# Kernel optimization log

Hardware: AMD Instinct MI355X
Metric: run time of the kernel (lower is better)

## Reference

```python
import jax, jax.numpy as jnp
import numpy as np

N = 50000       # nodes
E = 1600000     # directed edges (avg degree 32)
H = 2           # heads (layers 1-2)
F_IN = 128
F_HID = 64      # per-head hidden channels
F_OUT = 64
SCALE = 0.05


def setup_inputs() -> dict:
    key = jax.random.key(0)
    ks = jax.random.split(key, 15)

    def p(k, shape):
        return jax.random.normal(k, shape, jnp.float32) * SCALE

    x = jax.random.normal(ks[0], (N, F_IN), jnp.float32)
    edge_index = jax.random.randint(ks[1], (2, E), 0, N, dtype=jnp.int64)
    return dict(
        x=x,
        W1=p(ks[2], (F_IN, H * F_HID)), as1=p(ks[3], (H, F_HID)), ad1=p(ks[4], (H, F_HID)), b1=p(ks[5], (H * F_HID,)),
        W2=p(ks[6], (H * F_HID, H * F_HID)), as2=p(ks[7], (H, F_HID)), ad2=p(ks[8], (H, F_HID)), b2=p(ks[9], (H * F_HID,)),
        W3=p(ks[10], (H * F_HID, F_OUT)), as3=p(ks[11], (1, F_OUT)), ad3=p(ks[12], (1, F_OUT)), b3=p(ks[13], (F_OUT,)),
        edge_index=edge_index,
    )


def gat_layer(x, W, a_src, a_dst, b, src, dst, heads, f_out):
    """One PyG-style GATConv (concat=True, negative_slope=0.2), dropout off (eval)."""
    n = x.shape[0]
    h = (x @ W).reshape(n, heads, f_out)                 # [N,H,F]
    al_s = jnp.einsum('nhf,hf->nh', h, a_src)            # (x_j * att_src).sum(-1)
    al_d = jnp.einsum('nhf,hf->nh', h, a_dst)
    e = jax.nn.leaky_relu(al_s[src] + al_d[dst], 0.2)    # [Etot,H]
    # segment softmax over incoming edges of each dst node
    m = jax.lax.stop_gradient(jax.ops.segment_max(e, dst, num_segments=n))
    ee = jnp.exp(e - m[dst])
    denom = jax.ops.segment_sum(ee, dst, num_segments=n)
    alpha = ee / (denom[dst] + 1e-16)                    # [Etot,H]
    out = jax.ops.segment_sum(h[src] * alpha[:, :, None], dst, num_segments=n)
    return out.reshape(n, heads * f_out) + b


def reference(x, W1, as1, ad1, b1, W2, as2, ad2, b2, W3, as3, ad3, b3, edge_index):
    # add_self_loops=True (PyG default): same augmented edge set for all layers
    loops = jnp.arange(N, dtype=edge_index.dtype)
    src = jnp.concatenate([edge_index[0], loops])
    dst = jnp.concatenate([edge_index[1], loops])
    h = jax.nn.elu(gat_layer(x, W1, as1, ad1, b1, src, dst, H, F_HID))
    h = jax.nn.elu(gat_layer(h, W2, as2, ad2, b2, src, dst, H, F_HID))
    h = jax.nn.elu(gat_layer(h, W3, as3, ad3, b3, src, dst, 1, F_OUT))
    return h
```

## Files before the change

kernel.cpp:

```cpp
#include <hip/hip_runtime.h>
#include <hip/hip_bf16.h>
#include <hip/hip_fp16.h>


#define ELU(x) ((x) > 0.f ? (x) : (__expf(x) - 1.f))
#define BSH 8
#define CHK 8192

typedef _Float16 f16x8 __attribute__((ext_vector_type(8)));
typedef float    f32x4 __attribute__((ext_vector_type(4)));
typedef float    f32x2 __attribute__((ext_vector_type(2)));

__device__ inline unsigned int f16x4_to_fp8(__half2 h0, __half2 h1) {
    float2 a = __half22float2(h0), b = __half22float2(h1);
    unsigned int r = __builtin_amdgcn_cvt_pk_fp8_f32(a.x, a.y, 0, false);
    r = __builtin_amdgcn_cvt_pk_fp8_f32(b.x, b.y, r, true);
    return r;
}

__global__ __launch_bounds__(256) void phase0(
    const float* __restrict__ W1, __half* __restrict__ Wt1,
    const float* __restrict__ W2, __half* __restrict__ Wt2,
    const float* __restrict__ W3, __half* __restrict__ Wt3,
    const int* __restrict__ ei, int* __restrict__ bhist_rows, int E_)
{
    const int t = threadIdx.x;
    const int b = blockIdx.x;
    if (b < 160) {
        const float* W; __half* Wt; int N, base;
        if (b < 64)       { W = W1; Wt = Wt1; N = 128; base = b; }
        else if (b < 128) { W = W2; Wt = Wt2; N = 128; base = b - 64; }
        else              { W = W3; Wt = Wt3; N = 64;  base = b - 128; }
        int idx = base * 256 + t;
        if (idx < N * 128) {
            int nn = idx >> 7, k = idx & 127;
            Wt[idx] = __float2half(W[k * N + nn]);
        }
    } else {
        __shared__ int cnt[256];
        int hb = b - 160;
        cnt[t] = 0;
        __syncthreads();
        const int e0 = hb * CHK;
        for (int i = t; i < CHK; i += 256) {
            int e = e0 + i;
            if (e >= E_) break;
            atomicAdd(&cnt[ei[E_ + e] >> BSH], 1);
        }
        __syncthreads();
        bhist_rows[hb * 256 + t] = cnt[t];
    }
}

__global__ __launch_bounds__(256) void scan_bases(
    const int* __restrict__ bhist_rows, int* __restrict__ boff,
    int* __restrict__ bases, int* __restrict__ part, int HB, int n, int NB)
{
    __shared__ int tot[256];
    __shared__ int col[256];
    const int t = threadIdx.x;
    const int b = blockIdx.x;

    int v = 0;
    for (int r = 0; r < HB; r++) v += bhist_rows[r * 256 + t];
    int nodes_t = n - (t << BSH);
    nodes_t = nodes_t < 0 ? 0 : (nodes_t > 256 ? 256 : nodes_t);
    v = (t < NB) ? (v + nodes_t) : 0;
    tot[t] = v;
    __syncthreads();
    for (int d = 1; d < 256; d <<= 1) {
        int x = (t >= d) ? tot[t - d] : 0;
        __syncthreads();
        tot[t] += x;
        __syncthreads();
    }
    if (b == 0) {
        if (t < NB) boff[t + 1] = tot[t];
        if (t == 0) boff[0] = 0;
    }
    const int base0 = (b > 0) ? tot[b - 1] : 0;
    const int bend  = tot[b];

    int c = (t < HB) ? bhist_rows[t * 256 + b] : 0;
    col[t] = c;
    __syncthreads();
    for (int d = 1; d < 256; d <<= 1) {
        int x = (t >= d) ? col[t - d] : 0;
        __syncthreads();
        col[t] += x;
        __syncthreads();
    }
    if (t < HB) bases[b * HB + t] = base0 + col[t] - c;

    const int n0 = b << BSH;
    const int nodes = min(256, n - n0);
    const int sl0 = bend - nodes;
    if (t < nodes) part[sl0 + t] = (n0 + t) | (t << 16);
}

__global__ __launch_bounds__(256) void edge_partition(
    const int* __restrict__ ei, const int* __restrict__ bases,
    int* __restrict__ part, int E_, int HB, int NB)
{
    __shared__ int cnt[256];
    __shared__ int sbase[256];
    const int t = threadIdx.x;
    const int hb = blockIdx.x;
    cnt[t] = 0;
    sbase[t] = (t < NB) ? bases[t * HB + hb] : 0;
    __syncthreads();
    const int e0 = hb * CHK;
    for (int i = t; i < CHK; i += 256) {
        int e = e0 + i;
        if (e >= E_) break;
        int src = ei[e], dst = ei[E_ + e];
        int b = dst >> BSH;
        int pos = sbase[b] + atomicAdd(&cnt[b], 1);
        part[pos] = src | ((dst & 255) << 16);
    }
}

__global__ __launch_bounds__(256) void bucket_fill(
    const int* __restrict__ boff, const int* __restrict__ part,
    int* __restrict__ csr, int* __restrict__ off, int n)
{
    __shared__ int sm[256];
    __shared__ int cur[256];
    __shared__ int slice[12544];
    const int t = threadIdx.x;
    const int b = blockIdx.x;
    const int n0 = b << BSH;
    const int nodes = min(256, n - n0);
    const int off0 = boff[b];
    const int sz = boff[b + 1] - off0;

    cur[t] = 0;
    __syncthreads();
    for (int i = t; i < sz; i += 256)
        atomicAdd(&cur[(part[off0 + i] >> 16) & 255], 1);
    __syncthreads();
    int v = cur[t];
    sm[t] = v;
    __syncthreads();
    for (int d = 1; d < 256; d <<= 1) {
        int x = (t >= d) ? sm[t - d] : 0;
        __syncthreads();
        sm[t] += x;
        __syncthreads();
    }
    const int excl = sm[t] - v;
    if (t < nodes) off[n0 + t] = off0 + excl;
    if (t == nodes - 1) off[n0 + nodes] = off0 + sz;
    cur[t] = excl;
    __syncthreads();

    if (sz <= 12544) {
        for (int i = t; i < sz; i += 256) {
            int p  = part[off0 + i];
            int dl = (p >> 16) & 255;
            int pos = atomicAdd(&cur[dl], 1);
            slice[pos] = p & 0xFFFF;
        }
        __syncthreads();
        for (int i = t; i < sz; i += 256)
            csr[off0 + i] = slice[i];
    } else {
        for (int i = t; i < sz; i += 256) {
            int p  = part[off0 + i];
            int dl = (p >> 16) & 255;
            int pos = atomicAdd(&cur[dl], 1);
            csr[off0 + pos] = p & 0xFFFF;
        }
    }
}

__global__ __launch_bounds__(256) void gemm1_mfma(
    const float* __restrict__ A, const __half* __restrict__ Wt,
    unsigned char* __restrict__ Hout, const float* __restrict__ a_s,
    const float* __restrict__ a_d, float* __restrict__ alS,
    float* __restrict__ alD, int nrows)
{
    constexpr int N = 128, NT = 8, WR = 136;
    __shared__ _Float16 wt[N * WR];
    __shared__ _Float16 hst[4][16 * WR];

    const int t = threadIdx.x, w = t >> 6, l = t & 63;
    const int q = l >> 4, n = l & 15;
    const int node0 = blockIdx.x * 64;
    const int row_base = node0 + w * 16;

    for (int i = t; i < N * 16; i += 256) {
        int r = i >> 4, c = i & 15;
        float4 v = *(const float4*)&Wt[r * 128 + c * 8];
        *(float4*)&wt[r * WR + c * 8] = v;
    }
    __syncthreads();

    f32x4 acc[NT];
#pragma unroll
    for (int ct = 0; ct < NT; ct++) acc[ct] = (f32x4){0.f, 0.f, 0.f, 0.f};

    int arow = row_base + n; if (arow >= nrows) arow = nrows - 1;
    const float* Ap = A + (size_t)arow * 128 + q * 8;
#pragma unroll
    for (int ks = 0; ks < 4; ks++) {
        float4 va = *(const float4*)(Ap + ks * 32);
        float4 vb = *(const float4*)(Ap + ks * 32 + 4);
        f16x8 a = { (_Float16)va.x, (_Float16)va.y, (_Float16)va.z, (_Float16)va.w,
                    (_Float16)vb.x, (_Float16)vb.y, (_Float16)vb.z, (_Float16)vb.w };
#pragma unroll
        for (int ct = 0; ct < NT; ct++) {
            f16x8 bb = *(const f16x8*)&wt[(ct * 16 + n) * WR + ks * 32 + q * 8];
            acc[ct] = __builtin_amdgcn_mfma_f32_16x16x32_f16(a, bb, acc[ct], 0, 0, 0);
        }
    }

    float asv[NT], adv[NT];
#pragma unroll
    for (int ct = 0; ct < NT; ct++) {
        asv[ct] = a_s[ct * 16 + n];
        adv[ct] = a_d[ct * 16 + n];
    }
#pragma unroll
    for (int r = 0; r < 4; r++) {
        int grow = row_base + q * 4 + r;
        float s0 = 0.f, d0 = 0.f, s1 = 0.f, d1 = 0.f;
#pragma unroll
        for (int ct = 0; ct < NT; ct++) {
            float v = acc[ct][r];
            float ps = v * asv[ct], pd = v * adv[ct];
            if (ct >= 4) { s1 += ps; d1 += pd; }
            else         { s0 += ps; d0 += pd; }
        }
#pragma unroll
        for (int m = 1; m < 16; m <<= 1) {
            s0 += __shfl_xor(s0, m); d0 += __shfl_xor(d0, m);
            s1 += __shfl_xor(s1, m); d1 += __shfl_xor(d1, m);
        }
        if (n == 0 && grow < nrows) {
            alS[grow * 2] = s0;     alD[grow * 2] = d0;
            alS[grow * 2 + 1] = s1; alD[grow * 2 + 1] = d1;
        }
    }

#pragma unroll
    for (int ct = 0; ct < NT; ct++)
#pragma unroll
        for (int r = 0; r < 4; r++)
            hst[w][(q * 4 + r) * WR + ct * 16 + n] = (_Float16)acc[ct][r];
    __syncthreads();
    {
        int row = l >> 2, c = l & 3;
        int grow = row_base + row;
        if (grow < nrows) {
#pragma unroll
            for (int i = 0; i < 4; i++) {
                float4 v = *(float4*)&hst[w][row * WR + c * 32 + i * 8];
                const __half2* hp = (const __half2*)&v;
                uint2 o;
                o.x = f16x4_to_fp8(hp[0], hp[1]);
                o.y = f16x4_to_fp8(hp[2], hp[3]);
                *(uint2*)&Hout[(size_t)grow * 128 + c * 32 + i * 8] = o;
            }
        }
    }
}

template<int OUTN>
__global__ __launch_bounds__(256) void gat_gather_gemm(
    const int* __restrict__ off, const int* __restrict__ csr,
    const unsigned char* __restrict__ h, const float* __restrict__ alS,
    const float* __restrict__ alD, const float* __restrict__ bias,
    const __half* __restrict__ Wt, const float* __restrict__ a_s,
    const float* __restrict__ a_d, unsigned char* __restrict__ Hout,
    float* __restrict__ alSo, float* __restrict__ alDo, int n)
{
    constexpr int H = 2, HF = 128, WR = 136;
    constexpr int CTW = OUTN / 64;
    constexpr int CPW = OUTN / 4;
    __shared__ _Float16 actT[16 * WR];
    __shared__ float red_s[4][16], red_d[4][16];

    const int t = threadIdx.x;
    const int node0 = blockIdx.x * 16;

    const int l = t & 15;
    const int node = node0 + (t >> 4);
    const bool valid = node < n;
    const int c0 = l * 8;
    const int head = c0 >> 6;
    const int nodec = valid ? node : (n - 1);
    const float ad = alD[nodec * H + head];
    int s0 = 0, s1 = 1;
    if (valid) { s0 = off[node]; s1 = off[node + 1]; }
    const int last = s1 - 1;
    float a0 = 0.f, a1 = 0.f, a2 = 0.f, a3 = 0.f;
    float a4 = 0.f, a5 = 0.f, a6 = 0.f, a7 = 0.f, wsum = 0.f;

    float as[4];
    uint2 v[4];
    {
        int srcs[4];
#pragma unroll
        for (int k = 0; k < 4; k++) {
            int j = s0 + k;
            srcs[k] = csr[j <= last ? j : last];
        }
#pragma unroll
        for (int k = 0; k < 4; k++) {
            as[k] = alS[srcs[k] * H + head];
            v[k]  = *(const uint2*)&h[(size_t)srcs[k] * HF + c0];
        }
    }
    for (int j = s0; j < s1; j += 4) {
        int nsrc[4];
#pragma unroll
        for (int k = 0; k < 4; k++) {
            int jj = j + 4 + k;
            nsrc[k] = csr[jj <= last ? jj : last];
        }
        float nas[4];
        uint2 nv[4];
#pragma unroll
        for (int k = 0; k < 4; k++) {
            nas[k] = alS[nsrc[k] * H + head];
            nv[k]  = *(const uint2*)&h[(size_t)nsrc[k] * HF + c0];
        }
#pragma unroll
        for (int k = 0; k < 4; k++) {
            float s = as[k] + ad;
            s = s > 0.f ? s : 0.2f * s;
            float w = __expf(s);
            w = (j + k <= last) ? w : 0.f;
            f32x2 f0 = __builtin_amdgcn_cvt_pk_f32_fp8(v[k].x, false);
            f32x2 f1 = __builtin_amdgcn_cvt_pk_f32_fp8(v[k].x, true);
            f32x2 f2 = __builtin_amdgcn_cvt_pk_f32_fp8(v[k].y, false);
            f32x2 f3 = __builtin_amdgcn_cvt_pk_f32_fp8(v[k].y, true);
            a0 = fmaf(w, f0.x, a0); a1 = fmaf(w, f0.y, a1);
            a2 = fmaf(w, f1.x, a2); a3 = fmaf(w, f1.y, a3);
            a4 = fmaf(w, f2.x, a4); a5 = fmaf(w, f2.y, a5);
            a6 = fmaf(w, f3.x, a6); a7 = fmaf(w, f3.y, a7);
            wsum += w;
        }
#pragma unroll
        for (int k = 0; k < 4; k++) { as[k] = nas[k]; v[k] = nv[k]; }
    }
    {
        const float inv = 1.f / (wsum + 1e-16f);
        float4 b0 = *(const float4*)&bias[c0];
        float4 b1 = *(const float4*)&bias[c0 + 4];
        float o[8];
        o[0] = ELU(fmaf(a0, inv, b0.x));
        o[1] = ELU(fmaf(a1, inv, b0.y));
        o[2] = ELU(fmaf(a2, inv, b0.z));
        o[3] = ELU(fmaf(a3, inv, b0.w));
        o[4] = ELU(fmaf(a4, inv, b1.x));
        o[5] = ELU(fmaf(a5, inv, b1.y));
        o[6] = ELU(fmaf(a6, inv, b1.z));
        o[7] = ELU(fmaf(a7, inv, b1.w));
        __half2 p[4];
#pragma unroll
        for (int k = 0; k < 4; k++) p[k] = __floats2half2_rn(o[2 * k], o[2 * k + 1]);
        *(float4*)&actT[(t >> 4) * WR + l * 8] = *(float4*)p;
    }
    __syncthreads();

    const int w = t >> 6, l64 = t & 63, q = l64 >> 4, nn = l64 & 15;
    const __half* Wp = Wt + (w * CPW + nn) * 128 + q * 8;
    f32x4 acc[CTW];
#pragma unroll
    for (int ct = 0; ct < CTW; ct++) acc[ct] = (f32x4){0.f, 0.f, 0.f, 0.f};
#pragma unroll
    for (int ks = 0; ks < 4; ks++) {
        f16x8 a = *(const f16x8*)&actT[nn * WR + ks * 32 + q * 8];
#pragma unroll
        for (int ct = 0; ct < CTW; ct++) {
            f16x8 bb = *(const f16x8*)(Wp + ct * 16 * 128 + ks * 32);
            acc[ct] = __builtin_amdgcn_mfma_f32_16x16x32_f16(a, bb, acc[ct], 0, 0, 0);
        }
    }

    float asv[CTW], adv[CTW];
#pragma unroll
    for (int ct = 0; ct < CTW; ct++) {
        asv[ct] = a_s[w * CPW + ct * 16 + nn];
        adv[ct] = a_d[w * CPW + ct * 16 + nn];
    }
#pragma unroll
    for (int r = 0; r < 4; r++) {
        float s = 0.f, d = 0.f;
#pragma unroll
        for (int ct = 0; ct < CTW; ct++) {
            float vv = acc[ct][r];
            s = fmaf(vv, asv[ct], s);
            d = fmaf(vv, adv[ct], d);
        }
#pragma unroll
        for (int m = 1; m < 16; m <<= 1) {
            s += __shfl_xor(s, m);
            d += __shfl_xor(d, m);
        }
        if (nn == 0) { red_s[w][q * 4 + r] = s; red_d[w][q * 4 + r] = d; }
    }
    __syncthreads();

#pragma unroll
    for (int ct = 0; ct < CTW; ct++)
#pragma unroll
        for (int r = 0; r < 4; r++)
            actT[(q * 4 + r) * WR + w * CPW + ct * 16 + nn] = (_Float16)acc[ct][r];
    if (OUTN == 128) {
        if (t < 32) {
            int m = t & 15, hh = t >> 4;
            int grow = node0 + m;
            if (grow < n) {
                alSo[grow * 2 + hh] = red_s[2 * hh][m] + red_s[2 * hh + 1][m];
                alDo[grow * 2 + hh] = red_d[2 * hh][m] + red_d[2 * hh + 1][m];
            }
        }
    } else {
        if (t < 16) {
            int grow = node0 + t;
            if (grow < n) {
                alSo[grow] = red_s[0][t] + red_s[1][t] + red_s[2][t] + red_s[3][t];
                alDo[grow] = red_d[0][t] + red_d[1][t] + red_d[2][t] + red_d[3][t];
            }
        }
    }
    __syncthreads();

    if (OUTN == 128) {
        int row = t >> 4, c = t & 15;
        int grow = node0 + row;
        if (grow < n) {
            float4 v8 = *(float4*)&actT[row * WR + c * 8];
            const __half2* hp = (const __half2*)&v8;
            uint2 o;
            o.x = f16x4_to_fp8(hp[0], hp[1]);
            o.y = f16x4_to_fp8(hp[2], hp[3]);
            *(uint2*)&Hout[(size_t)grow * 128 + c * 8] = o;
        }
    } else {
        if (t < 128) {
            int row = t >> 3, c = t & 7;
            int grow = node0 + row;
            if (grow < n) {
                float4 v8 = *(float4*)&actT[row * WR + c * 8];
                const __half2* hp = (const __half2*)&v8;
                uint2 o;
                o.x = f16x4_to_fp8(hp[0], hp[1]);
                o.y = f16x4_to_fp8(hp[2], hp[3]);
                *(uint2*)&Hout[(size_t)grow * 64 + c * 8] = o;
            }
        }
    }
}

__global__ __launch_bounds__(256) void gat_gather_out(
    const int* __restrict__ off, const int* __restrict__ csr,
    const unsigned char* __restrict__ h, const float* __restrict__ alS,
    const float* __restrict__ alD, const float* __restrict__ b,
    float* __restrict__ out, int n)
{
    constexpr int HF = 64, LPN = 8, NPB = 32;
    const int l    = threadIdx.x % LPN;
    const int node = blockIdx.x * NPB + threadIdx.x / LPN;
    if (node >= n) return;
    const int c0   = l * 8;
    const float ad = alD[node];

    const int s0 = off[node], s1 = off[node + 1];
    const int last = s1 - 1;
    float a0 = 0.f, a1 = 0.f, a2 = 0.f, a3 = 0.f;
    float a4 = 0.f, a5 = 0.f, a6 = 0.f, a7 = 0.f, wsum = 0.f;

    float as[4];
    uint2 v[4];
    {
        int srcs[4];
#pragma unroll
        for (int k = 0; k < 4; k++) {
            int j = s0 + k;
            srcs[k] = csr[j <= last ? j : last];
        }
#pragma unroll
        for (int k = 0; k < 4; k++) {
            as[k] = alS[srcs[k]];
            v[k]  = *(const uint2*)&h[(size_t)srcs[k] * HF + c0];
        }
    }
    for (int j = s0; j < s1; j += 4) {
        int nsrc[4];
#pragma unroll
        for (int k = 0; k < 4; k++) {
            int jj = j + 4 + k;
            nsrc[k] = csr[jj <= last ? jj : last];
        }
        float nas[4];
        uint2 nv[4];
#pragma unroll
        for (int k = 0; k < 4; k++) {
            nas[k] = alS[nsrc[k]];
            nv[k]  = *(const uint2*)&h[(size_t)nsrc[k] * HF + c0];
        }
#pragma unroll
        for (int k = 0; k < 4; k++) {
            float s = as[k] + ad;
            s = s > 0.f ? s : 0.2f * s;
            float w = __expf(s);
            w = (j + k <= last) ? w : 0.f;
            f32x2 f0 = __builtin_amdgcn_cvt_pk_f32_fp8(v[k].x, false);
            f32x2 f1 = __builtin_amdgcn_cvt_pk_f32_fp8(v[k].x, true);
            f32x2 f2 = __builtin_amdgcn_cvt_pk_f32_fp8(v[k].y, false);
            f32x2 f3 = __builtin_amdgcn_cvt_pk_f32_fp8(v[k].y, true);
            a0 = fmaf(w, f0.x, a0); a1 = fmaf(w, f0.y, a1);
            a2 = fmaf(w, f1.x, a2); a3 = fmaf(w, f1.y, a3);
            a4 = fmaf(w, f2.x, a4); a5 = fmaf(w, f2.y, a5);
            a6 = fmaf(w, f3.x, a6); a7 = fmaf(w, f3.y, a7);
            wsum += w;
        }
#pragma unroll
        for (int k = 0; k < 4; k++) { as[k] = nas[k]; v[k] = nv[k]; }
    }

    const float inv = 1.f / (wsum + 1e-16f);
    float4 b0 = *(const float4*)&b[c0];
    float4 b1 = *(const float4*)&b[c0 + 4];
    float4 o0, o1;
    o0.x = ELU(fmaf(a0, inv, b0.x));
    o0.y = ELU(fmaf(a1, inv, b0.y));
    o0.z = ELU(fmaf(a2, inv, b0.z));
    o0.w = ELU(fmaf(a3, inv, b0.w));
    o1.x = ELU(fmaf(a4, inv, b1.x));
    o1.y = ELU(fmaf(a5, inv, b1.y));
    o1.z = ELU(fmaf(a6, inv, b1.z));
    o1.w = ELU(fmaf(a7, inv, b1.w));
    *(float4*)&out[(size_t)node * HF + c0]     = o0;
    *(float4*)&out[(size_t)node * HF + c0 + 4] = o1;
}

extern "C" void kernel_launch(void* const* d_in, const int* in_sizes, int n_in,
                              void* d_out, int out_size, void* d_ws, size_t ws_size,
                              hipStream_t stream)
{
    const float* x   = (const float*)d_in[0];
    const float* W1  = (const float*)d_in[1];
    const float* as1 = (const float*)d_in[2];
    const float* ad1 = (const float*)d_in[3];
    const float* b1  = (const float*)d_in[4];
    const float* W2  = (const float*)d_in[5];
    const float* as2 = (const float*)d_in[6];
    const float* ad2 = (const float*)d_in[7];
    const float* b2  = (const float*)d_in[8];
    const float* W3  = (const float*)d_in[9];
    const float* as3 = (const float*)d_in[10];
    const float* ad3 = (const float*)d_in[11];
    const float* b3  = (const float*)d_in[12];
    const int*   ei  = (const int*)d_in[13];
    float* out = (float*)d_out;

    const int N_   = in_sizes[0] / 128;
    const int E_   = in_sizes[13] / 2;
    const int Etot = E_ + N_;
    const int NB   = (N_ + 255) >> BSH;
    const int HB   = (E_ + CHK - 1) / CHK;

    char* ws = (char*)d_ws;
    size_t o = 0;
    auto alloc = [&](size_t bytes) { void* p = ws + o; o += (bytes + 255) & ~255ull; return p; };
    unsigned char* h1 = (unsigned char*)alloc((size_t)N_ * 128);
    unsigned char* h2 = (unsigned char*)alloc((size_t)N_ * 128);
    unsigned char* h3 = (unsigned char*)alloc((size_t)N_ * 64);
    __half* Wt1   = (__half*)alloc((size_t)128 * 128 * 2);
    __half* Wt2   = (__half*)alloc((size_t)128 * 128 * 2);
    __half* Wt3   = (__half*)alloc((size_t)64 * 128 * 2);
    float* alSa   = (float*)alloc((size_t)N_ * 2 * 4);
    float* alDa   = (float*)alloc((size_t)N_ * 2 * 4);
    float* alSb   = (float*)alloc((size_t)N_ * 2 * 4);
    float* alDb   = (float*)alloc((size_t)N_ * 2 * 4);
    int*   offb   = (int*)alloc((size_t)(N_ + 1) * 4);
    int*   bhrows = (int*)alloc((size_t)HB * 256 * 4);
    int*   boff   = (int*)alloc((size_t)257 * 4);
    int*   bases  = (int*)alloc((size_t)256 * HB * 4);
    int*   part   = (int*)alloc((size_t)Etot * 4);
    int*   csr    = (int*)alloc((size_t)Etot * 4);

    const dim3 blk(256);

    phase0<<<160 + HB, blk, 0, stream>>>(W1, Wt1, W2, Wt2, W3, Wt3, ei, bhrows, E_);
    scan_bases<<<NB, blk, 0, stream>>>(bhrows, boff, bases, part, HB, N_, NB);
    edge_partition<<<HB, blk, 0, stream>>>(ei, bases, part, E_, HB, NB);
    bucket_fill<<<NB, blk, 0, stream>>>(boff, part, csr, offb, N_);

    gemm1_mfma<<<(N_ + 63) / 64, blk, 0, stream>>>(x, Wt1, h1, as1, ad1, alSa, alDa, N_);
    gat_gather_gemm<128><<<(N_ + 15) / 16, blk, 0, stream>>>(
        offb, csr, h1, alSa, alDa, b1, Wt2, as2, ad2, h2, alSb, alDb, N_);
    gat_gather_gemm<64><<<(N_ + 15) / 16, blk, 0, stream>>>(
        offb, csr, h2, alSb, alDb, b2, Wt3, as3, ad3, h3, alSa, alDa, N_);
    gat_gather_out<<<(N_ + 31) / 32, blk, 0, stream>>>(
        offb, csr, h3, alSa, alDa, b3, out, N_);
}
```

Before: 294.1 us.

## Share edge metadata loads and attention weights across lanes via shuffles

In both gather kernels, each lane of a node's lane group now loads one CSR entry and its source attention score, computes the leaky-ReLU exp weight once, and broadcasts index and weight to the other lanes with width-limited shuffles. Before, every lane redundantly loaded all CSR indices and alS values and recomputed the exp per edge. The edge loop now advances 16 (or 8) edges per iteration with prefetch of the next batch's metadata, and the feature gathers are issued in groups of 8 (or 4). This cuts redundant scalar loads and transcendental work, at the cost of shuffle instructions and extra masked iterations for low-degree nodes.

```diff
diff --git a/kernel.cpp b/kernel.cpp
--- a/kernel.cpp
+++ b/kernel.cpp
@@ -275,7 +275,7 @@
     const float* __restrict__ a_d, unsigned char* __restrict__ Hout,
     float* __restrict__ alSo, float* __restrict__ alDo, int n)
 {
-    constexpr int H = 2, HF = 128, WR = 136;
+    constexpr int HF = 128, WR = 136;
     constexpr int CTW = OUTN / 64;
     constexpr int CPW = OUTN / 4;
     __shared__ _Float16 actT[16 * WR];
@@ -288,62 +288,63 @@
     const int node = node0 + (t >> 4);
     const bool valid = node < n;
     const int c0 = l * 8;
-    const int head = c0 >> 6;
+    const int head = l >> 3;
     const int nodec = valid ? node : (n - 1);
-    const float ad = alD[nodec * H + head];
+    const float2 adv = *(const float2*)&alD[nodec * 2];
     int s0 = 0, s1 = 1;
     if (valid) { s0 = off[node]; s1 = off[node + 1]; }
     const int last = s1 - 1;
     float a0 = 0.f, a1 = 0.f, a2 = 0.f, a3 = 0.f;
     float a4 = 0.f, a5 = 0.f, a6 = 0.f, a7 = 0.f, wsum = 0.f;
 
-    float as[4];
-    uint2 v[4];
-    {
-        int srcs[4];
-#pragma unroll
-        for (int k = 0; k < 4; k++) {
-            int j = s0 + k;
-            srcs[k] = csr[j <= last ? j : last];
-        }
-#pragma unroll
-        for (int k = 0; k < 4; k++) {
-            as[k] = alS[srcs[k] * H + head];
-            v[k]  = *(const uint2*)&h[(size_t)srcs[k] * HF + c0];
-        }
-    }
-    for (int j = s0; j < s1; j += 4) {
-        int nsrc[4];
-#pragma unroll
-        for (int k = 0; k < 4; k++) {
-            int jj = j + 4 + k;
-            nsrc[k] = csr[jj <= last ? jj : last];
-        }
-        float nas[4];
-        uint2 nv[4];
-#pragma unroll
-        for (int k = 0; k < 4; k++) {
-            nas[k] = alS[nsrc[k] * H + head];
-            nv[k]  = *(const uint2*)&h[(size_t)nsrc[k] * HF + c0];
-        }
-#pragma unroll
-        for (int k = 0; k < 4; k++) {
-            float s = as[k] + ad;
-            s = s > 0.f ? s : 0.2f * s;
-            float w = __expf(s);
-            w = (j + k <= last) ? w : 0.f;
-            f32x2 f0 = __builtin_amdgcn_cvt_pk_f32_fp8(v[k].x, false);
-            f32x2 f1 = __builtin_amdgcn_cvt_pk_f32_fp8(v[k].x, true);
-            f32x2 f2 = __builtin_amdgcn_cvt_pk_f32_fp8(v[k].y, false);
-            f32x2 f3 = __builtin_amdgcn_cvt_pk_f32_fp8(v[k].y, true);
-            a0 = fmaf(w, f0.x, a0); a1 = fmaf(w, f0.y, a1);
-            a2 = fmaf(w, f1.x, a2); a3 = fmaf(w, f1.y, a3);
-            a4 = fmaf(w, f2.x, a4); a5 = fmaf(w, f2.y, a5);
-            a6 = fmaf(w, f3.x, a6); a7 = fmaf(w, f3.y, a7);
-            wsum += w;
-        }
-#pragma unroll
-        for (int k = 0; k < 4; k++) { as[k] = nas[k]; v[k] = nv[k]; }
+    int msrc; float mw0, mw1;
+    auto load_meta = [&](int j, int& src, float& w0, float& w1) {
+        int jj = j + l;
+        bool ok = jj <= last;
+        src = csr[ok ? jj : last];
+        float2 as2 = *(const float2*)&alS[src * 2];
+        float e0 = as2.x + adv.x; e0 = e0 > 0.f ? e0 : 0.2f * e0;
+        float e1 = as2.y + adv.y; e1 = e1 > 0.f ? e1 : 0.2f * e1;
+        w0 = ok ? __expf(e0) : 0.f;
+        w1 = ok ? __expf(e1) : 0.f;
+    };
+    load_meta(s0, msrc, mw0, mw1);
+
+    for (int j = s0; j < s1; j += 16) {
+        int nsrc; float nw0, nw1;
+        load_meta(j + 16, nsrc, nw0, nw1);
+
+        auto consume8 = [&](int kbase) {
+            int sk[8]; float wk[8];
+#pragma unroll
+            for (int k = 0; k < 8; k++) {
+                int kk = kbase + k;
+                sk[k] = __shfl(msrc, kk, 16);
+                float wa = __shfl(mw0, kk, 16);
+                float wb = __shfl(mw1, kk, 16);
+                wk[k] = head ? wb : wa;
+            }
+            uint2 hv[8];
+#pragma unroll
+            for (int k = 0; k < 8; k++)
+                hv[k] = *(const uint2*)&h[(size_t)sk[k] * HF + c0];
+#pragma unroll
+            for (int k = 0; k < 8; k++) {
+                float w = wk[k];
+                f32x2 f0 = __builtin_amdgcn_cvt_pk_f32_fp8(hv[k].x, false);
+                f32x2 f1 = __builtin_amdgcn_cvt_pk_f32_fp8(hv[k].x, true);
+                f32x2 f2 = __builtin_amdgcn_cvt_pk_f32_fp8(hv[k].y, false);
+                f32x2 f3 = __builtin_amdgcn_cvt_pk_f32_fp8(hv[k].y, true);
+                a0 = fmaf(w, f0.x, a0); a1 = fmaf(w, f0.y, a1);
+                a2 = fmaf(w, f1.x, a2); a3 = fmaf(w, f1.y, a3);
+                a4 = fmaf(w, f2.x, a4); a5 = fmaf(w, f2.y, a5);
+                a6 = fmaf(w, f3.x, a6); a7 = fmaf(w, f3.y, a7);
+                wsum += w;
+            }
+        };
+        consume8(0);
+        if (j + 8 <= last) consume8(8);
+        msrc = nsrc; mw0 = nw0; mw1 = nw1;
     }
     {
         const float inv = 1.f / (wsum + 1e-16f);
@@ -380,11 +381,11 @@
         }
     }
 
-    float asv[CTW], adv[CTW];
+    float asv[CTW], adv2[CTW];
 #pragma unroll
     for (int ct = 0; ct < CTW; ct++) {
-        asv[ct] = a_s[w * CPW + ct * 16 + nn];
-        adv[ct] = a_d[w * CPW + ct * 16 + nn];
+        asv[ct]  = a_s[w * CPW + ct * 16 + nn];
+        adv2[ct] = a_d[w * CPW + ct * 16 + nn];
     }
 #pragma unroll
     for (int r = 0; r < 4; r++) {
@@ -393,7 +394,7 @@
         for (int ct = 0; ct < CTW; ct++) {
             float vv = acc[ct][r];
             s = fmaf(vv, asv[ct], s);
-            d = fmaf(vv, adv[ct], d);
+            d = fmaf(vv, adv2[ct], d);
         }
 #pragma unroll
         for (int m = 1; m < 16; m <<= 1) {
@@ -474,53 +475,48 @@
     float a0 = 0.f, a1 = 0.f, a2 = 0.f, a3 = 0.f;
     float a4 = 0.f, a5 = 0.f, a6 = 0.f, a7 = 0.f, wsum = 0.f;
 
-    float as[4];
-    uint2 v[4];
-    {
-        int srcs[4];
-#pragma unroll
-        for (int k = 0; k < 4; k++) {
-            int j = s0 + k;
-            srcs[k] = csr[j <= last ? j : last];
-        }
-#pragma unroll
-        for (int k = 0; k < 4; k++) {
-            as[k] = alS[srcs[k]];
-            v[k]  = *(const uint2*)&h[(size_t)srcs[k] * HF + c0];
-        }
-    }
-    for (int j = s0; j < s1; j += 4) {
-        int nsrc[4];
-#pragma unroll
-        for (int k = 0; k < 4; k++) {
-            int jj = j + 4 + k;
-            nsrc[k] = csr[jj <= last ? jj : last];
-        }
-        float nas[4];
-        uint2 nv[4];
-#pragma unroll
-        for (int k = 0; k < 4; k++) {
-            nas[k] = alS[nsrc[k]];
-            nv[k]  = *(const uint2*)&h[(size_t)nsrc[k] * HF + c0];
-        }
-#pragma unroll
-        for (int k = 0; k < 4; k++) {
-            float s = as[k] + ad;
-            s = s > 0.f ? s : 0.2f * s;
-            float w = __expf(s);
-            w = (j + k <= last) ? w : 0.f;
-            f32x2 f0 = __builtin_amdgcn_cvt_pk_f32_fp8(v[k].x, false);
-            f32x2 f1 = __builtin_amdgcn_cvt_pk_f32_fp8(v[k].x, true);
-            f32x2 f2 = __builtin_amdgcn_cvt_pk_f32_fp8(v[k].y, false);
-            f32x2 f3 = __builtin_amdgcn_cvt_pk_f32_fp8(v[k].y, true);
-            a0 = fmaf(w, f0.x, a0); a1 = fmaf(w, f0.y, a1);
-            a2 = fmaf(w, f1.x, a2); a3 = fmaf(w, f1.y, a3);
-            a4 = fmaf(w, f2.x, a4); a5 = fmaf(w, f2.y, a5);
-            a6 = fmaf(w, f3.x, a6); a7 = fmaf(w, f3.y, a7);
-            wsum += w;
-        }
-#pragma unroll
-        for (int k = 0; k < 4; k++) { as[k] = nas[k]; v[k] = nv[k]; }
+    int msrc; float mw;
+    auto load_meta = [&](int j, int& src, float& w) {
+        int jj = j + l;
+        bool ok = jj <= last;
+        src = csr[ok ? jj : last];
+        float e = alS[src] + ad; e = e > 0.f ? e : 0.2f * e;
+        w = ok ? __expf(e) : 0.f;
+    };
+    load_meta(s0, msrc, mw);
+
+    for (int j = s0; j < s1; j += 8) {
+        int nsrc; float nw;
+        load_meta(j + 8, nsrc, nw);
+
+        auto consume4 = [&](int kbase) {
+            int sk[4]; float wk[4];
+#pragma unroll
+            for (int k = 0; k < 4; k++) {
+                sk[k] = __shfl(msrc, kbase + k, 8);
+                wk[k] = __shfl(mw,   kbase + k, 8);
+            }
+            uint2 hv[4];
+#pragma unroll
+            for (int k = 0; k < 4; k++)
+                hv[k] = *(const uint2*)&h[(size_t)sk[k] * HF + c0];
+#pragma unroll
+            for (int k = 0; k < 4; k++) {
+                float w = wk[k];
+                f32x2 f0 = __builtin_amdgcn_cvt_pk_f32_fp8(hv[k].x, false);
+                f32x2 f1 = __builtin_amdgcn_cvt_pk_f32_fp8(hv[k].x, true);
+                f32x2 f2 = __builtin_amdgcn_cvt_pk_f32_fp8(hv[k].y, false);
+                f32x2 f3 = __builtin_amdgcn_cvt_pk_f32_fp8(hv[k].y, true);
+                a0 = fmaf(w, f0.x, a0); a1 = fmaf(w, f0.y, a1);
+                a2 = fmaf(w, f1.x, a2); a3 = fmaf(w, f1.y, a3);
+                a4 = fmaf(w, f2.x, a4); a5 = fmaf(w, f2.y, a5);
+                a6 = fmaf(w, f3.x, a6); a7 = fmaf(w, f3.y, a7);
+                wsum += w;
+            }
+        };
+        consume4(0);
+        if (j + 4 <= last) consume4(4);
+        msrc = nsrc; mw = nw;
     }
 
     const float inv = 1.f / (wsum + 1e-16f);
```

Result: no change. 299.6 us (+1.9%).

## Fuse layer-1 GEMM into edge partition launch and widen per-lane gather vectors

Applied to the files above, without the earlier changes.

Merges the edge-partition kernel and the first-layer MFMA GEMM into one launch, with blocks split by blockIdx, so the two independent jobs run concurrently and one launch is dropped. The gather kernels now assign 16 fp8 channels per lane using 128-bit loads instead of 8 channels with 64-bit loads. Each gather-GEMM block handles 32 nodes instead of 16, and its four waves are remapped over a 2x2 row/column tile. The software prefetch depth drops from 4 to 2 edges, which lowers memory-level parallelism per lane, and the merged kernel's shared-memory union is sized for the GEMM, which may reduce occupancy for the partition blocks.

```diff
diff --git a/kernel.cpp b/kernel.cpp
--- a/kernel.cpp
+++ b/kernel.cpp
@@ -98,25 +98,119 @@
     if (t < nodes) part[sl0 + t] = (n0 + t) | (t << 16);
 }
 
-__global__ __launch_bounds__(256) void edge_partition(
+__global__ __launch_bounds__(256) void partition_gemm1(
     const int* __restrict__ ei, const int* __restrict__ bases,
-    int* __restrict__ part, int E_, int HB, int NB)
+    int* __restrict__ part, int E_, int HB, int NB,
+    const float* __restrict__ A, const __half* __restrict__ Wt,
+    unsigned char* __restrict__ Hout, const float* __restrict__ a_s,
+    const float* __restrict__ a_d, float* __restrict__ alS,
+    float* __restrict__ alD, int nrows)
 {
-    __shared__ int cnt[256];
-    __shared__ int sbase[256];
+    __shared__ union SM {
+        struct { int cnt[256]; int sbase[256]; } p;
+        struct { _Float16 wt[128 * 136]; _Float16 hst[4][16 * 136]; } g;
+    } sm;
     const int t = threadIdx.x;
-    const int hb = blockIdx.x;
-    cnt[t] = 0;
-    sbase[t] = (t < NB) ? bases[t * HB + hb] : 0;
-    __syncthreads();
-    const int e0 = hb * CHK;
-    for (int i = t; i < CHK; i += 256) {
-        int e = e0 + i;
-        if (e >= E_) break;
-        int src = ei[e], dst = ei[E_ + e];
-        int b = dst >> BSH;
-        int pos = sbase[b] + atomicAdd(&cnt[b], 1);
-        part[pos] = src | ((dst & 255) << 16);
+
+    if (blockIdx.x < HB) {
+        const int hb = blockIdx.x;
+        sm.p.cnt[t] = 0;
+        sm.p.sbase[t] = (t < NB) ? bases[t * HB + hb] : 0;
+        __syncthreads();
+        const int e0 = hb * CHK;
+        for (int i = t; i < CHK; i += 256) {
+            int e = e0 + i;
+            if (e >= E_) break;
+            int src = ei[e], dst = ei[E_ + e];
+            int b = dst >> BSH;
+            int pos = sm.p.sbase[b] + atomicAdd(&sm.p.cnt[b], 1);
+            part[pos] = src | ((dst & 255) << 16);
+        }
+        return;
+    }
+
+    constexpr int N = 128, NT = 8, WR = 136;
+    _Float16* wt = sm.g.wt;
+
+    const int w = t >> 6, l = t & 63;
+    const int q = l >> 4, nn1 = l & 15;
+    const int node0 = (blockIdx.x - HB) * 64;
+    const int row_base = node0 + w * 16;
+
+    for (int i = t; i < N * 16; i += 256) {
+        int r = i >> 4, c = i & 15;
+        float4 v = *(const float4*)&Wt[r * 128 + c * 8];
+        *(float4*)&wt[r * WR + c * 8] = v;
+    }
+    __syncthreads();
+
+    f32x4 acc[NT];
+#pragma unroll
+    for (int ct = 0; ct < NT; ct++) acc[ct] = (f32x4){0.f, 0.f, 0.f, 0.f};
+
+    int arow = row_base + nn1; if (arow >= nrows) arow = nrows - 1;
+    const float* Ap = A + (size_t)arow * 128 + q * 8;
+#pragma unroll
+    for (int ks = 0; ks < 4; ks++) {
+        float4 va = *(const float4*)(Ap + ks * 32);
+        float4 vb = *(const float4*)(Ap + ks * 32 + 4);
+        f16x8 a = { (_Float16)va.x, (_Float16)va.y, (_Float16)va.z, (_Float16)va.w,
+                    (_Float16)vb.x, (_Float16)vb.y, (_Float16)vb.z, (_Float16)vb.w };
+#pragma unroll
+        for (int ct = 0; ct < NT; ct++) {
+            f16x8 bb = *(const f16x8*)&wt[(ct * 16 + nn1) * WR + ks * 32 + q * 8];
+            acc[ct] = __builtin_amdgcn_mfma_f32_16x16x32_f16(a, bb, acc[ct], 0, 0, 0);
+        }
+    }
+
+    float asv[NT], adv[NT];
+#pragma unroll
+    for (int ct = 0; ct < NT; ct++) {
+        asv[ct] = a_s[ct * 16 + nn1];
+        adv[ct] = a_d[ct * 16 + nn1];
+    }
+#pragma unroll
+    for (int r = 0; r < 4; r++) {
+        int grow = row_base + q * 4 + r;
+        float s0 = 0.f, d0 = 0.f, s1 = 0.f, d1 = 0.f;
+#pragma unroll
+        for (int ct = 0; ct < NT; ct++) {
+            float v = acc[ct][r];
+            float ps = v * asv[ct], pd = v * adv[ct];
+            if (ct >= 4) { s1 += ps; d1 += pd; }
+            else         { s0 += ps; d0 += pd; }
+        }
+#pragma unroll
+        for (int m = 1; m < 16; m <<= 1) {
+            s0 += __shfl_xor(s0, m); d0 += __shfl_xor(d0, m);
+            s1 += __shfl_xor(s1, m); d1 += __shfl_xor(d1, m);
+        }
+        if (nn1 == 0 && grow < nrows) {
+            alS[grow * 2] = s0;     alD[grow * 2] = d0;
+            alS[grow * 2 + 1] = s1; alD[grow * 2 + 1] = d1;
+        }
+    }
+
+#pragma unroll
+    for (int ct = 0; ct < NT; ct++)
+#pragma unroll
+        for (int r = 0; r < 4; r++)
+            sm.g.hst[w][(q * 4 + r) * WR + ct * 16 + nn1] = (_Float16)acc[ct][r];
+    __syncthreads();
+    {
+        int row = l >> 2, c = l & 3;
+        int grow = row_base + row;
+        if (grow < nrows) {
+#pragma unroll
+            for (int i = 0; i < 4; i++) {
+                float4 v = *(float4*)&sm.g.hst[w][row * WR + c * 32 + i * 8];
+                const __half2* hp = (const __half2*)&v;
+                uint2 o;
+                o.x = f16x4_to_fp8(hp[0], hp[1]);
+                o.y = f16x4_to_fp8(hp[2], hp[3]);
+                *(uint2*)&Hout[(size_t)grow * 128 + c * 32 + i * 8] = o;
+            }
+        }
     }
 }
 
@@ -174,98 +268,6 @@
     }
 }
 
-__global__ __launch_bounds__(256) void gemm1_mfma(
-    const float* __restrict__ A, const __half* __restrict__ Wt,
-    unsigned char* __restrict__ Hout, const float* __restrict__ a_s,
-    const float* __restrict__ a_d, float* __restrict__ alS,
-    float* __restrict__ alD, int nrows)
-{
-    constexpr int N = 128, NT = 8, WR = 136;
-    __shared__ _Float16 wt[N * WR];
-    __shared__ _Float16 hst[4][16 * WR];
-
-    const int t = threadIdx.x, w = t >> 6, l = t & 63;
-    const int q = l >> 4, n = l & 15;
-    const int node0 = blockIdx.x * 64;
-    const int row_base = node0 + w * 16;
-
-    for (int i = t; i < N * 16; i += 256) {
-        int r = i >> 4, c = i & 15;
-        float4 v = *(const float4*)&Wt[r * 128 + c * 8];
-        *(float4*)&wt[r * WR + c * 8] = v;
-    }
-    __syncthreads();
-
-    f32x4 acc[NT];
-#pragma unroll
-    for (int ct = 0; ct < NT; ct++) acc[ct] = (f32x4){0.f, 0.f, 0.f, 0.f};
-
-    int arow = row_base + n; if (arow >= nrows) arow = nrows - 1;
-    const float* Ap = A + (size_t)arow * 128 + q * 8;
-#pragma unroll
-    for (int ks = 0; ks < 4; ks++) {
-        float4 va = *(const float4*)(Ap + ks * 32);
-        float4 vb = *(const float4*)(Ap + ks * 32 + 4);
-        f16x8 a = { (_Float16)va.x, (_Float16)va.y, (_Float16)va.z, (_Float16)va.w,
-                    (_Float16)vb.x, (_Float16)vb.y, (_Float16)vb.z, (_Float16)vb.w };
-#pragma unroll
-        for (int ct = 0; ct < NT; ct++) {
-            f16x8 bb = *(const f16x8*)&wt[(ct * 16 + n) * WR + ks * 32 + q * 8];
-            acc[ct] = __builtin_amdgcn_mfma_f32_16x16x32_f16(a, bb, acc[ct], 0, 0, 0);
-        }
-    }
-
-    float asv[NT], adv[NT];
-#pragma unroll
-    for (int ct = 0; ct < NT; ct++) {
-        asv[ct] = a_s[ct * 16 + n];
-        adv[ct] = a_d[ct * 16 + n];
-    }
-#pragma unroll
-    for (int r = 0; r < 4; r++) {
-        int grow = row_base + q * 4 + r;
-        float s0 = 0.f, d0 = 0.f, s1 = 0.f, d1 = 0.f;
-#pragma unroll
-        for (int ct = 0; ct < NT; ct++) {
-            float v = acc[ct][r];
-            float ps = v * asv[ct], pd = v * adv[ct];
-            if (ct >= 4) { s1 += ps; d1 += pd; }
-            else         { s0 += ps; d0 += pd; }
-        }
-#pragma unroll
-        for (int m = 1; m < 16; m <<= 1) {
-            s0 += __shfl_xor(s0, m); d0 += __shfl_xor(d0, m);
-            s1 += __shfl_xor(s1, m); d1 += __shfl_xor(d1, m);
-        }
-        if (n == 0 && grow < nrows) {
-            alS[grow * 2] = s0;     alD[grow * 2] = d0;
-            alS[grow * 2 + 1] = s1; alD[grow * 2 + 1] = d1;
-        }
-    }
-
-#pragma unroll
-    for (int ct = 0; ct < NT; ct++)
-#pragma unroll
-        for (int r = 0; r < 4; r++)
-            hst[w][(q * 4 + r) * WR + ct * 16 + n] = (_Float16)acc[ct][r];
-    __syncthreads();
-    {
-        int row = l >> 2, c = l & 3;
-        int grow = row_base + row;
-        if (grow < nrows) {
-#pragma unroll
-            for (int i = 0; i < 4; i++) {
-                float4 v = *(float4*)&hst[w][row * WR + c * 32 + i * 8];
-                const __half2* hp = (const __half2*)&v;
-                uint2 o;
-                o.x = f16x4_to_fp8(hp[0], hp[1]);
-                o.y = f16x4_to_fp8(hp[2], hp[3]);
-                *(uint2*)&Hout[(size_t)grow * 128 + c * 32 + i * 8] = o;
-            }
-        }
-    }
-}
-
 template<int OUTN>
 __global__ __launch_bounds__(256) void gat_gather_gemm(
     const int* __restrict__ off, const int* __restrict__ csr,
@@ -275,116 +277,122 @@
     const float* __restrict__ a_d, unsigned char* __restrict__ Hout,
     float* __restrict__ alSo, float* __restrict__ alDo, int n)
 {
-    constexpr int H = 2, HF = 128, WR = 136;
-    constexpr int CTW = OUTN / 64;
-    constexpr int CPW = OUTN / 4;
-    __shared__ _Float16 actT[16 * WR];
+    constexpr int HF = 128, WR = 136;
+    constexpr int CTW = OUTN / 32;
+    __shared__ _Float16 actT[32 * WR];
     __shared__ float red_s[4][16], red_d[4][16];
 
     const int t = threadIdx.x;
-    const int node0 = blockIdx.x * 16;
-
-    const int l = t & 15;
-    const int node = node0 + (t >> 4);
+    const int node0 = blockIdx.x * 32;
+
+    const int l = t & 7;
+    const int nl = t >> 3;
+    const int node = node0 + nl;
     const bool valid = node < n;
-    const int c0 = l * 8;
-    const int head = c0 >> 6;
+    const int c0 = l * 16;
+    const int head = l >> 2;
     const int nodec = valid ? node : (n - 1);
-    const float ad = alD[nodec * H + head];
+    const float ad = alD[nodec * 2 + head];
     int s0 = 0, s1 = 1;
     if (valid) { s0 = off[node]; s1 = off[node + 1]; }
     const int last = s1 - 1;
-    float a0 = 0.f, a1 = 0.f, a2 = 0.f, a3 = 0.f;
-    float a4 = 0.f, a5 = 0.f, a6 = 0.f, a7 = 0.f, wsum = 0.f;
-
-    float as[4];
-    uint2 v[4];
+
+    float a[16];
+#pragma unroll
+    for (int i = 0; i < 16; i++) a[i] = 0.f;
+    float wsum = 0.f;
+
+    float as[2]; uint4 v[2];
     {
-        int srcs[4];
-#pragma unroll
-        for (int k = 0; k < 4; k++) {
+        int srcs[2];
+#pragma unroll
+        for (int k = 0; k < 2; k++) {
             int j = s0 + k;
             srcs[k] = csr[j <= last ? j : last];
         }
 #pragma unroll
-        for (int k = 0; k < 4; k++) {
-            as[k] = alS[srcs[k] * H + head];
-            v[k]  = *(const uint2*)&h[(size_t)srcs[k] * HF + c0];
-        }
-    }
-    for (int j = s0; j < s1; j += 4) {
-        int nsrc[4];
-#pragma unroll
-        for (int k = 0; k < 4; k++) {
-            int jj = j + 4 + k;
+        for (int k = 0; k < 2; k++) {
+            as[k] = alS[srcs[k] * 2 + head];
+            v[k]  = *(const uint4*)&h[(size_t)srcs[k] * HF + c0];
+        }
+    }
+    for (int j = s0; j < s1; j += 2) {
+        int nsrc[2];
+#pragma unroll
+        for (int k = 0; k < 2; k++) {
+            int jj = j + 2 + k;
             nsrc[k] = csr[jj <= last ? jj : last];
         }
-        float nas[4];
-        uint2 nv[4];
-#pragma unroll
-        for (int k = 0; k < 4; k++) {
-            nas[k] = alS[nsrc[k] * H + head];
-            nv[k]  = *(const uint2*)&h[(size_t)nsrc[k] * HF + c0];
-        }
-#pragma unroll
-        for (int k = 0; k < 4; k++) {
+        float nas[2]; uint4 nv[2];
+#pragma unroll
+        for (int k = 0; k < 2; k++) {
+            nas[k] = alS[nsrc[k] * 2 + head];
+            nv[k]  = *(const uint4*)&h[(size_t)nsrc[k] * HF + c0];
+        }
+#pragma unroll
+        for (int k = 0; k < 2; k++) {
             float s = as[k] + ad;
             s = s > 0.f ? s : 0.2f * s;
             float w = __expf(s);
             w = (j + k <= last) ? w : 0.f;
-            f32x2 f0 = __builtin_amdgcn_cvt_pk_f32_fp8(v[k].x, false);
-            f32x2 f1 = __builtin_amdgcn_cvt_pk_f32_fp8(v[k].x, true);
-            f32x2 f2 = __builtin_amdgcn_cvt_pk_f32_fp8(v[k].y, false);
-            f32x2 f3 = __builtin_amdgcn_cvt_pk_f32_fp8(v[k].y, true);
-            a0 = fmaf(w, f0.x, a0); a1 = fmaf(w, f0.y, a1);
-            a2 = fmaf(w, f1.x, a2); a3 = fmaf(w, f1.y, a3);
-            a4 = fmaf(w, f2.x, a4); a5 = fmaf(w, f2.y, a5);
-            a6 = fmaf(w, f3.x, a6); a7 = fmaf(w, f3.y, a7);
+            unsigned int dw[4] = { v[k].x, v[k].y, v[k].z, v[k].w };
+#pragma unroll
+            for (int d = 0; d < 4; d++) {
+                f32x2 lo = __builtin_amdgcn_cvt_pk_f32_fp8(dw[d], false);
+                f32x2 hi = __builtin_amdgcn_cvt_pk_f32_fp8(dw[d], true);
+                a[d * 4 + 0] = fmaf(w, lo.x, a[d * 4 + 0]);
+                a[d * 4 + 1] = fmaf(w, lo.y, a[d * 4 + 1]);
+                a[d * 4 + 2] = fmaf(w, hi.x, a[d * 4 + 2]);
+                a[d * 4 + 3] = fmaf(w, hi.y, a[d * 4 + 3]);
+            }
             wsum += w;
         }
 #pragma unroll
-        for (int k = 0; k < 4; k++) { as[k] = nas[k]; v[k] = nv[k]; }
+        for (int k = 0; k < 2; k++) { as[k] = nas[k]; v[k] = nv[k]; }
     }
     {
         const float inv = 1.f / (wsum + 1e-16f);
-        float4 b0 = *(const float4*)&bias[c0];
-        float4 b1 = *(const float4*)&bias[c0 + 4];
-        float o[8];
-        o[0] = ELU(fmaf(a0, inv, b0.x));
-        o[1] = ELU(fmaf(a1, inv, b0.y));
-        o[2] = ELU(fmaf(a2, inv, b0.z));
-        o[3] = ELU(fmaf(a3, inv, b0.w));
-        o[4] = ELU(fmaf(a4, inv, b1.x));
-        o[5] = ELU(fmaf(a5, inv, b1.y));
-        o[6] = ELU(fmaf(a6, inv, b1.z));
-        o[7] = ELU(fmaf(a7, inv, b1.w));
-        __half2 p[4];
-#pragma unroll
-        for (int k = 0; k < 4; k++) p[k] = __floats2half2_rn(o[2 * k], o[2 * k + 1]);
-        *(float4*)&actT[(t >> 4) * WR + l * 8] = *(float4*)p;
+        float bb[16];
+        *(float4*)&bb[0]  = *(const float4*)&bias[c0];
+        *(float4*)&bb[4]  = *(const float4*)&bias[c0 + 4];
+        *(float4*)&bb[8]  = *(const float4*)&bias[c0 + 8];
+        *(float4*)&bb[12] = *(const float4*)&bias[c0 + 12];
+        __half2 p[8];
+#pragma unroll
+        for (int i = 0; i < 8; i++) {
+            float o0 = ELU(fmaf(a[2 * i],     inv, bb[2 * i]));
+            float o1 = ELU(fmaf(a[2 * i + 1], inv, bb[2 * i + 1]));
+            p[i] = __floats2half2_rn(o0, o1);
+        }
+        *(float4*)&actT[nl * WR + c0]     = *(float4*)&p[0];
+        *(float4*)&actT[nl * WR + c0 + 8] = *(float4*)&p[4];
     }
     __syncthreads();
 
     const int w = t >> 6, l64 = t & 63, q = l64 >> 4, nn = l64 & 15;
-    const __half* Wp = Wt + (w * CPW + nn) * 128 + q * 8;
+    const int rt = w & 1;
+    const int ch = w >> 1;
+    const int rbase = rt * 16;
+    const int cbase = ch * (OUTN / 2);
+    const __half* Wp = Wt + (size_t)(cbase + nn) * 128 + q * 8;
     f32x4 acc[CTW];
 #pragma unroll
     for (int ct = 0; ct < CTW; ct++) acc[ct] = (f32x4){0.f, 0.f, 0.f, 0.f};
 #pragma unroll
     for (int ks = 0; ks < 4; ks++) {
-        f16x8 a = *(const f16x8*)&actT[nn * WR + ks * 32 + q * 8];
+        f16x8 af = *(const f16x8*)&actT[(rbase + nn) * WR + ks * 32 + q * 8];
 #pragma unroll
         for (int ct = 0; ct < CTW; ct++) {
             f16x8 bb = *(const f16x8*)(Wp + ct * 16 * 128 + ks * 32);
-            acc[ct] = __builtin_amdgcn_mfma_f32_16x16x32_f16(a, bb, acc[ct], 0, 0, 0);
-        }
-    }
-
-    float asv[CTW], adv[CTW];
+            acc[ct] = __builtin_amdgcn_mfma_f32_16x16x32_f16(af, bb, acc[ct], 0, 0, 0);
+        }
+    }
+
+    float asv[CTW], adv2[CTW];
 #pragma unroll
     for (int ct = 0; ct < CTW; ct++) {
-        asv[ct] = a_s[w * CPW + ct * 16 + nn];
-        adv[ct] = a_d[w * CPW + ct * 16 + nn];
+        asv[ct]  = a_s[cbase + ct * 16 + nn];
+        adv2[ct] = a_d[cbase + ct * 16 + nn];
     }
 #pragma unroll
     for (int r = 0; r < 4; r++) {
@@ -393,7 +401,7 @@
         for (int ct = 0; ct < CTW; ct++) {
             float vv = acc[ct][r];
             s = fmaf(vv, asv[ct], s);
-            d = fmaf(vv, adv[ct], d);
+            d = fmaf(vv, adv2[ct], d);
         }
 #pragma unroll
         for (int m = 1; m < 16; m <<= 1) {
@@ -408,50 +416,54 @@
     for (int ct = 0; ct < CTW; ct++)
 #pragma unroll
         for (int r = 0; r < 4; r++)
-            actT[(q * 4 + r) * WR + w * CPW + ct * 16 + nn] = (_Float16)acc[ct][r];
+            actT[(rbase + q * 4 + r) * WR + cbase + ct * 16 + nn] = (_Float16)acc[ct][r];
+
     if (OUTN == 128) {
+        if (t < 64) {
+            int i = t & 15, ww = t >> 4;
+            int grow = node0 + (ww & 1) * 16 + i;
+            if (grow < n) {
+                alSo[grow * 2 + (ww >> 1)] = red_s[ww][i];
+                alDo[grow * 2 + (ww >> 1)] = red_d[ww][i];
+            }
+        }
+    } else {
         if (t < 32) {
-            int m = t & 15, hh = t >> 4;
-            int grow = node0 + m;
+            int i = t & 15, rt2 = t >> 4;
+            int grow = node0 + rt2 * 16 + i;
             if (grow < n) {
-                alSo[grow * 2 + hh] = red_s[2 * hh][m] + red_s[2 * hh + 1][m];
-                alDo[grow * 2 + hh] = red_d[2 * hh][m] + red_d[2 * hh + 1][m];
+                alSo[grow] = red_s[rt2][i] + red_s[rt2 + 2][i];
+                alDo[grow] = red_d[rt2][i] + red_d[rt2 + 2][i];
             }
         }
-    } else {
-        if (t < 16) {
-            int grow = node0 + t;
-            if (grow < n) {
-                alSo[grow] = red_s[0][t] + red_s[1][t] + red_s[2][t] + red_s[3][t];
-                alDo[grow] = red_d[0][t] + red_d[1][t] + red_d[2][t] + red_d[3][t];
-            }
-        }
     }
     __syncthreads();
 
     if (OUTN == 128) {
-        int row = t >> 4, c = t & 15;
+        int row = t >> 3, c = t & 7;
         int grow = node0 + row;
         if (grow < n) {
-            float4 v8 = *(float4*)&actT[row * WR + c * 8];
-            const __half2* hp = (const __half2*)&v8;
+            float4 p0 = *(float4*)&actT[row * WR + c * 16];
+            float4 p1 = *(float4*)&actT[row * WR + c * 16 + 8];
+            const __half2* h0 = (const __half2*)&p0;
+            const __half2* h1 = (const __half2*)&p1;
+            uint4 o;
+            o.x = f16x4_to_fp8(h0[0], h0[1]);
+            o.y = f16x4_to_fp8(h0[2], h0[3]);
+            o.z = f16x4_to_fp8(h1[0], h1[1]);
+            o.w = f16x4_to_fp8(h1[2], h1[3]);
+            *(uint4*)&Hout[(size_t)grow * 128 + c * 16] = o;
+        }
+    } else {
+        int row = t >> 3, c = t & 7;
+        int grow = node0 + row;
+        if (grow < n) {
+            float4 p0 = *(float4*)&actT[row * WR + c * 8];
+            const __half2* hp = (const __half2*)&p0;
             uint2 o;
             o.x = f16x4_to_fp8(hp[0], hp[1]);
             o.y = f16x4_to_fp8(hp[2], hp[3]);
-            *(uint2*)&Hout[(size_t)grow * 128 + c * 8] = o;
-        }
-    } else {
-        if (t < 128) {
-            int row = t >> 3, c = t & 7;
-            int grow = node0 + row;
-            if (grow < n) {
-                float4 v8 = *(float4*)&actT[row * WR + c * 8];
-                const __half2* hp = (const __half2*)&v8;
-                uint2 o;
-                o.x = f16x4_to_fp8(hp[0], hp[1]);
-                o.y = f16x4_to_fp8(hp[2], hp[3]);
-                *(uint2*)&Hout[(size_t)grow * 64 + c * 8] = o;
-            }
+            *(uint2*)&Hout[(size_t)grow * 64 + c * 8] = o;
         }
     }
 }
@@ -462,81 +474,87 @@
     const float* __restrict__ alD, const float* __restrict__ b,
     float* __restrict__ out, int n)
 {
-    constexpr int HF = 64, LPN = 8, NPB = 32;
-    const int l    = threadIdx.x % LPN;
-    const int node = blockIdx.x * NPB + threadIdx.x / LPN;
+    constexpr int HF = 64;
+    const int l    = threadIdx.x & 3;
+    const int node = blockIdx.x * 64 + (threadIdx.x >> 2);
     if (node >= n) return;
-    const int c0   = l * 8;
+    const int c0   = l * 16;
     const float ad = alD[node];
 
     const int s0 = off[node], s1 = off[node + 1];
     const int last = s1 - 1;
-    float a0 = 0.f, a1 = 0.f, a2 = 0.f, a3 = 0.f;
-    float a4 = 0.f, a5 = 0.f, a6 = 0.f, a7 = 0.f, wsum = 0.f;
-
-    float as[4];
-    uint2 v[4];
+
+    float a[16];
+#pragma unroll
+    for (int i = 0; i < 16; i++) a[i] = 0.f;
+    float wsum = 0.f;
+
+    float as[2]; uint4 v[2];
     {
-        int srcs[4];
-#pragma unroll
-        for (int k = 0; k < 4; k++) {
+        int srcs[2];
+#pragma unroll
+        for (int k = 0; k < 2; k++) {
             int j = s0 + k;
             srcs[k] = csr[j <= last ? j : last];
         }
 #pragma unroll
-        for (int k = 0; k < 4; k++) {
+        for (int k = 0; k < 2; k++) {
             as[k] = alS[srcs[k]];
-            v[k]  = *(const uint2*)&h[(size_t)srcs[k] * HF + c0];
-        }
-    }
-    for (int j = s0; j < s1; j += 4) {
-        int nsrc[4];
-#pragma unroll
-        for (int k = 0; k < 4; k++) {
-            int jj = j + 4 + k;
+            v[k]  = *(const uint4*)&h[(size_t)srcs[k] * HF + c0];
+        }
+    }
+    for (int j = s0; j < s1; j += 2) {
+        int nsrc[2];
+#pragma unroll
+        for (int k = 0; k < 2; k++) {
+            int jj = j + 2 + k;
             nsrc[k] = csr[jj <= last ? jj : last];
         }
-        float nas[4];
-        uint2 nv[4];
-#pragma unroll
-        for (int k = 0; k < 4; k++) {
+        float nas[2]; uint4 nv[2];
+#pragma unroll
+        for (int k = 0; k < 2; k++) {
             nas[k] = alS[nsrc[k]];
-            nv[k]  = *(const uint2*)&h[(size_t)nsrc[k] * HF + c0];
-        }
-#pragma unroll
-        for (int k = 0; k < 4; k++) {
+            nv[k]  = *(const uint4*)&h[(size_t)nsrc[k] * HF + c0];
+        }
+#pragma unroll
+        for (int k = 0; k < 2; k++) {
             float s = as[k] + ad;
             s = s > 0.f ? s : 0.2f * s;
             float w = __expf(s);
             w = (j + k <= last) ? w : 0.f;
-            f32x2 f0 = __builtin_amdgcn_cvt_pk_f32_fp8(v[k].x, false);
-            f32x2 f1 = __builtin_amdgcn_cvt_pk_f32_fp8(v[k].x, true);
-            f32x2 f2 = __builtin_amdgcn_cvt_pk_f32_fp8(v[k].y, false);
-            f32x2 f3 = __builtin_amdgcn_cvt_pk_f32_fp8(v[k].y, true);
-            a0 = fmaf(w, f0.x, a0); a1 = fmaf(w, f0.y, a1);
-            a2 = fmaf(w, f1.x, a2); a3 = fmaf(w, f1.y, a3);
-            a4 = fmaf(w, f2.x, a4); a5 = fmaf(w, f2.y, a5);
-            a6 = fmaf(w, f3.x, a6); a7 = fmaf(w, f3.y, a7);
+            unsigned int dw[4] = { v[k].x, v[k].y, v[k].z, v[k].w };
+#pragma unroll
+            for (int d = 0; d < 4; d++) {
+                f32x2 lo = __builtin_amdgcn_cvt_pk_f32_fp8(dw[d], false);
+                f32x2 hi = __builtin_amdgcn_cvt_pk_f32_fp8(dw[d], true);
+                a[d * 4 + 0] = fmaf(w, lo.x, a[d * 4 + 0]);
+                a[d * 4 + 1] = fmaf(w, lo.y, a[d * 4 + 1]);
+                a[d * 4 + 2] = fmaf(w, hi.x, a[d * 4 + 2]);
+                a[d * 4 + 3] = fmaf(w, hi.y, a[d * 4 + 3]);
+            }
             wsum += w;
         }
 #pragma unroll
-        for (int k = 0; k < 4; k++) { as[k] = nas[k]; v[k] = nv[k]; }
+        for (int k = 0; k < 2; k++) { as[k] = nas[k]; v[k] = nv[k]; }
     }
 
     const float inv = 1.f / (wsum + 1e-16f);
-    float4 b0 = *(const float4*)&b[c0];
-    float4 b1 = *(const float4*)&b[c0 + 4];
-    float4 o0, o1;
-    o0.x = ELU(fmaf(a0, inv, b0.x));
-    o0.y = ELU(fmaf(a1, inv, b0.y));
-    o0.z = ELU(fmaf(a2, inv, b0.z));
-    o0.w = ELU(fmaf(a3, inv, b0.w));
-    o1.x = ELU(fmaf(a4, inv, b1.x));
-    o1.y = ELU(fmaf(a5, inv, b1.y));
-    o1.z = ELU(fmaf(a6, inv, b1.z));
-    o1.w = ELU(fmaf(a7, inv, b1.w));
-    *(float4*)&out[(size_t)node * HF + c0]     = o0;
-    *(float4*)&out[(size_t)node * HF + c0 + 4] = o1;
+    float bb[16];
+    *(float4*)&bb[0]  = *(const float4*)&b[c0];
+    *(float4*)&bb[4]  = *(const float4*)&b[c0 + 4];
+    *(float4*)&bb[8]  = *(const float4*)&b[c0 + 8];
+    *(float4*)&bb[12] = *(const float4*)&b[c0 + 12];
+    float4 o[4];
+#pragma unroll
+    for (int g = 0; g < 4; g++) {
+        o[g].x = ELU(fmaf(a[4 * g + 0], inv, bb[4 * g + 0]));
+        o[g].y = ELU(fmaf(a[4 * g + 1], inv, bb[4 * g + 1]));
+        o[g].z = ELU(fmaf(a[4 * g + 2], inv, bb[4 * g + 2]));
+        o[g].w = ELU(fmaf(a[4 * g + 3], inv, bb[4 * g + 3]));
+    }
+#pragma unroll
+    for (int g = 0; g < 4; g++)
+        *(float4*)&out[(size_t)node * HF + c0 + 4 * g] = o[g];
 }
 
 extern "C" void kernel_launch(void* const* d_in, const int* in_sizes, int n_in,
@@ -586,17 +604,19 @@
     int*   csr    = (int*)alloc((size_t)Etot * 4);
 
     const dim3 blk(256);
+    const int G1 = (N_ + 63) / 64;
 
     phase0<<<160 + HB, blk, 0, stream>>>(W1, Wt1, W2, Wt2, W3, Wt3, ei, bhrows, E_);
     scan_bases<<<NB, blk, 0, stream>>>(bhrows, boff, bases, part, HB, N_, NB);
-    edge_partition<<<HB, blk, 0, stream>>>(ei, bases, part, E_, HB, NB);
+    partition_gemm1<<<HB + G1, blk, 0, stream>>>(
+        ei, bases, part, E_, HB, NB,
+        x, Wt1, h1, as1, ad1, alSa, alDa, N_);
     bucket_fill<<<NB, blk, 0, stream>>>(boff, part, csr, offb, N_);
 
-    gemm1_mfma<<<(N_ + 63) / 64, blk, 0, stream>>>(x, Wt1, h1, as1, ad1, alSa, alDa, N_);
-    gat_gather_gemm<128><<<(N_ + 15) / 16, blk, 0, stream>>>(
+    gat_gather_gemm<128><<<(N_ + 31) / 32, blk, 0, stream>>>(
         offb, csr, h1, alSa, alDa, b1, Wt2, as2, ad2, h2, alSb, alDb, N_);
-    gat_gather_gemm<64><<<(N_ + 15) / 16, blk, 0, stream>>>(
+    gat_gather_gemm<64><<<(N_ + 31) / 32, blk, 0, stream>>>(
         offb, csr, h2, alSb, alDb, b2, Wt3, as3, ad3, h3, alSa, alDa, N_);
-    gat_gather_out<<<(N_ + 31) / 32, blk, 0, stream>>>(
+    gat_gather_out<<<(N_ + 63) / 64, blk, 0, stream>>>(
         offb, csr, h3, alSa, alDa, b3, out, N_);
 }
```

After: 305.0 us. +3.7%, slower.
